# Kernel optimization log

Measured on AMD Instinct MI355X. Metric: run time of the kernel, lower is better.

Reference implementation:

```python
import jax, jax.numpy as jnp
import numpy as np

PAST, FUT = 64, 16
SB = 2048
N = PAST + FUT  # 80
OUTP = 35       # sum(emb dims) + 3


def _pre(cat, num, emb0, emb1, emb2, W1, b1, W2, b2, W3, b3):
    # pre_processing: embeddings + last-3 numeric cols -> MLP -> concat target col
    e = jnp.concatenate([emb0[cat[:, 0]], emb1[cat[:, 1]], emb2[cat[:, 2]]], -1)
    o = jnp.concatenate([e, num], -1)                 # [n, 35]
    h = jax.nn.relu(o @ W1 + b1)
    h = jax.nn.relu(h @ W2 + b2)
    h = h @ W3 + b3                                   # [n, 34]
    return jnp.concatenate([h, num[:, -1:]], -1)      # [n, 35]


def _gcn(x, src, dst, W, b):
    n = x.shape[0]
    h = x @ W
    deg = 1.0 + jax.ops.segment_sum(jnp.ones(src.shape, x.dtype), dst, num_segments=n)
    dinv = jax.lax.rsqrt(deg)
    msg = h[src] * (dinv[src] * dinv[dst])[:, None]
    agg = jax.ops.segment_sum(msg, dst, num_segments=n) + h * (dinv * dinv)[:, None]
    return agg + b


def _forward(x1_cat, x1_num, x2_cat, x2_num, e1, e2,
             emb0, emb1, emb2, pW1, pb1, pW2, pb2, pW3, pb3,
             g1W1, g1b1, g1W2, g1b2, g2W1, g2b1, g2W2, g2b2,
             kerW, smoothing, M):
    # masked-softmax adjacency A = softmax(relu(M M^T) masked to lower-tri, axis=1)
    Araw = jax.nn.relu(M @ M.T)
    tril = jnp.tril(jnp.ones((N, N), Araw.dtype))
    A = jax.nn.softmax(jnp.where(tril == 0, -jnp.inf, Araw), axis=1)

    x = _pre(x1_cat, x1_num, emb0, emb1, emb2, pW1, pb1, pW2, pb2, pW3, pb3)   # [SB*PAST, 35]
    x2 = _pre(x2_cat, x2_num, emb0, emb1, emb2, pW1, pb1, pW2, pb2, pW3, pb3)
    x2 = x2.reshape(SB, FUT, OUTP)

    # gnn1: GCN(35->64) -> ReLU -> GCN(64->34)
    h = jax.nn.relu(_gcn(x, e1[0], e1[1], g1W1, g1b1))
    x1 = _gcn(h, e1[0], e1[1], g1W2, g1b2).reshape(SB, PAST, OUTP - 1)

    x_kernel = jnp.concatenate([x1, x2[:, :, :-1]], -2)        # [SB, N, 34]
    y_kernel = x.reshape(SB, PAST, OUTP)[:, :, -1:]            # [SB, PAST, 1]

    # Mahalanobis kernel attention
    theta = kerW @ kerW.T
    theta = (theta + theta.T) / 2
    x_p = x_kernel[:, :PAST, :]
    x_f = x_kernel[:, PAST:, :]
    diff = x_p[:, None, :, :] - x_f[:, :, None, :]             # [SB, FUT, PAST, 34]
    # diagonal of diff @ theta @ diff^T, computed directly
    alpha = jnp.einsum('bqpo,oO,bqpO->bqp', diff, theta, diff)
    alpha = -0.5 * alpha / (jax.nn.sigmoid(smoothing[0]) * 0.01)
    A_tmp = A[PAST:, :PAST]                                    # [FUT, PAST]
    alpha = jnp.where(A_tmp[None] == 0, -jnp.inf, alpha)
    alpha = jax.nn.softmax(alpha, -1)
    yh = jnp.einsum('bqp,bpo->bqo', alpha, y_kernel)           # [SB, FUT, 1]

    x2 = jnp.concatenate([x2[:, :, :-1], yh], -1)              # [SB, FUT, 35]
    # gnn2: GCN(35->64) -> ReLU -> GCN(64->1)
    h2 = jax.nn.relu(_gcn(x2.reshape(-1, OUTP), e2[0], e2[1], g2W1, g2b1))
    out = _gcn(h2, e2[0], e2[1], g2W2, g2b2).reshape(SB, FUT)

    # cdist over concatenated past+future features, via norm trick
    xa = jnp.concatenate([x.reshape(SB, PAST, OUTP), x2], -2)  # [SB, N, 35]
    sq = jnp.sum(xa * xa, -1)
    d2 = sq[:, :, None] + sq[:, None, :] - 2.0 * jnp.einsum('bnd,bmd->bnm', xa, xa)
    cd = jnp.sqrt(jnp.maximum(d2, 0.0))
    return out, cd, A


def setup_inputs():
    key = jax.random.key(0)
    ks = jax.random.split(key, 24)
    f32 = jnp.float32
    n1, n2 = SB * PAST, SB * FUT
    E1, E2 = n1 * 8, n2 * 8
    return {
        'x1_cat': jax.random.randint(ks[0], (n1, 3), 0, 7, dtype=jnp.int32),
        'x1_num': jax.random.normal(ks[1], (n1, 3), f32),
        'x2_cat': jax.random.randint(ks[2], (n2, 3), 0, 7, dtype=jnp.int32),
        'x2_num': jax.random.normal(ks[3], (n2, 3), f32),
        'edge_index1': jax.random.randint(ks[4], (2, E1), 0, n1, dtype=jnp.int32),
        'edge_index2': jax.random.randint(ks[5], (2, E2), 0, n2, dtype=jnp.int32),
        'emb0': jax.random.normal(ks[6], (24, 16), f32),
        'emb1': jax.random.normal(ks[7], (7, 8), f32),
        'emb2': jax.random.normal(ks[8], (12, 8), f32),
        'pre_W1': jax.random.normal(ks[9], (35, 128), f32) * 0.1,
        'pre_b1': jnp.zeros((128,), f32),
        'pre_W2': jax.random.normal(ks[10], (128, 128), f32) * 0.08,
        'pre_b2': jnp.zeros((128,), f32),
        'pre_W3': jax.random.normal(ks[11], (128, 34), f32) * 0.08,
        'pre_b3': jnp.zeros((34,), f32),
        'g1_W1': jax.random.normal(ks[12], (35, 64), f32) * 0.1,
        'g1_b1': jnp.zeros((64,), f32),
        'g1_W2': jax.random.normal(ks[13], (64, 34), f32) * 0.1,
        'g1_b2': jnp.zeros((34,), f32),
        'g2_W1': jax.random.normal(ks[14], (35, 64), f32) * 0.1,
        'g2_b1': jnp.zeros((64,), f32),
        'g2_W2': jax.random.normal(ks[15], (64, 1), f32) * 0.1,
        'g2_b2': jnp.zeros((1,), f32),
        'ker_W': jax.random.normal(ks[16], (34, 128), f32) * 0.1,
        'smoothing': jax.random.normal(ks[17], (1,), f32),
        'M': jax.random.normal(ks[18], (N, N // 3), f32) * 0.1,
    }


def reference(x1_cat, x1_num, x2_cat, x2_num, edge_index1, edge_index2,
              emb0, emb1, emb2, pre_W1, pre_b1, pre_W2, pre_b2, pre_W3, pre_b3,
              g1_W1, g1_b1, g1_W2, g1_b2, g2_W1, g2_b1, g2_W2, g2_b2,
              ker_W, smoothing, M):
    return _forward(x1_cat, x1_num, x2_cat, x2_num, edge_index1, edge_index2,
                    emb0, emb1, emb2, pre_W1, pre_b1, pre_W2, pre_b2, pre_W3, pre_b3,
                    g1_W1, g1_b1, g1_W2, g1_b2, g2_W1, g2_b1, g2_W2, g2_b2,
                    ker_W, smoothing, M)
```

## Files before the change

### kernel.cpp

```cpp
#include <hip/hip_runtime.h>
#include <math.h>

#define PASTN 64
#define FUTN 16
#define NN 80

typedef __attribute__((ext_vector_type(8))) short sh8;
typedef __attribute__((ext_vector_type(4))) float f32x4;

__device__ __forceinline__ unsigned short f2bf(float f) {
    unsigned int u = __float_as_uint(f);
    return (unsigned short)((u + 0x7FFFu + ((u >> 16) & 1u)) >> 16);
}
__device__ __forceinline__ float bf2f(unsigned short s) {
    return __uint_as_float(((unsigned int)s) << 16);
}

__global__ __launch_bounds__(256) void k_setup(const float* __restrict__ M, const float* __restrict__ kerW,
                                               const float* __restrict__ smoothing,
                                               float* __restrict__ A_ws, float* __restrict__ A_out,
                                               float* __restrict__ theta, float* __restrict__ scale)
{
    __shared__ float Ms[80 * 26];
    __shared__ float Ar[80 * 80];
    const int t = threadIdx.x;
    for (int i = t; i < 80 * 26; i += 256) Ms[i] = M[i];
    __syncthreads();
    for (int idx = t; idx < 6400; idx += 256) {
        int i = idx / 80, j = idx - 80 * i;
        float acc = 0.f;
#pragma unroll
        for (int k = 0; k < 26; ++k) acc = fmaf(Ms[i * 26 + k], Ms[j * 26 + k], acc);
        Ar[idx] = fmaxf(acc, 0.f);
    }
    __syncthreads();
    if (t < 80) {
        float mx = -1e30f;
        for (int j = 0; j <= t; ++j) mx = fmaxf(mx, Ar[t * 80 + j]);
        float s = 0.f;
        for (int j = 0; j <= t; ++j) s += expf(Ar[t * 80 + j] - mx);
        float inv = 1.f / s;
        for (int j = 0; j < 80; ++j) {
            float v = (j <= t) ? expf(Ar[t * 80 + j] - mx) * inv : 0.f;
            A_ws[t * 80 + j] = v;
            A_out[t * 80 + j] = v;
        }
    }
    for (int idx = t; idx < 34 * 34; idx += 256) {
        int i = idx / 34, j = idx - 34 * i;
        float acc = 0.f;
        for (int k = 0; k < 128; ++k) acc = fmaf(kerW[i * 128 + k], kerW[j * 128 + k], acc);
        theta[idx] = acc;
    }
    if (t == 0) {
        float s0 = smoothing[0];
        float sig = 1.f / (1.f + expf(-s0));
        scale[0] = -0.5f / (sig * 0.01f);
    }
}

__global__ void k_wconv(const float* __restrict__ W1, const float* __restrict__ W2,
                        const float* __restrict__ W3,
                        unsigned short* __restrict__ W1h, unsigned short* __restrict__ W1l,
                        unsigned short* __restrict__ W2h, unsigned short* __restrict__ W2l,
                        unsigned short* __restrict__ W3h, unsigned short* __restrict__ W3l)
{
    int g = blockIdx.x * 256 + threadIdx.x;
    float w;
    unsigned short *dh, *dl;
    int gi;
    if (g < 8192) {
        gi = g;
        int i = gi & 7, l = (gi >> 3) & 63, ks = (gi >> 9) & 1, nt = gi >> 10;
        int col = nt * 16 + (l & 15);
        int k = ks * 32 + ((l >> 4) << 3) + i;
        w = (k < 35) ? W1[k * 128 + col] : 0.f;
        dh = W1h; dl = W1l;
    } else if (g < 24576) {
        gi = g - 8192;
        int i = gi & 7, l = (gi >> 3) & 63, ks = (gi >> 9) & 3, nt = gi >> 11;
        int col = nt * 16 + (l & 15);
        int k = ks * 32 + ((l >> 4) << 3) + i;
        w = W2[k * 128 + col];
        dh = W2h; dl = W2l;
    } else {
        gi = g - 24576;
        int i = gi & 7, l = (gi >> 3) & 63, ks = (gi >> 9) & 3, nt = gi >> 11;
        int col = nt * 16 + (l & 15);
        int k = ks * 32 + ((l >> 4) << 3) + i;
        w = (col < 34) ? W3[k * 34 + col] : 0.f;
        dh = W3h; dl = W3l;
    }
    unsigned short hi = f2bf(w);
    dh[gi] = hi;
    dl[gi] = f2bf(w - bf2f(hi));
}

__global__ void k_deg2(const int* __restrict__ dst1, const int* __restrict__ dst2,
                       int* __restrict__ deg1, int* __restrict__ deg2,
                       int E1, int E2, int nbe1)
{
    int gb = blockIdx.x;
    if (gb < nbe1) {
        int e = gb * 256 + threadIdx.x;
        if (e < E1) atomicAdd(&deg1[dst1[e]], 1);
    } else {
        int e = (gb - nbe1) * 256 + threadIdx.x;
        if (e < E2) atomicAdd(&deg2[dst2[e]], 1);
    }
}

#define SCHUNK 1024
__global__ __launch_bounds__(256) void k_scan_reduce2(const int* __restrict__ deg1, const int* __restrict__ deg2,
                                                      int* __restrict__ bsumA, int* __restrict__ bsumB,
                                                      int n1, int n2, int nb1)
{
    __shared__ int sd[256];
    const int gb = blockIdx.x, t = threadIdx.x;
    const int which = (gb < nb1) ? 0 : 1;
    const int b = which ? gb - nb1 : gb;
    const int* deg = which ? deg2 : deg1;
    const int n = which ? n2 : n1;
    const int base = b * SCHUNK;
    int s = 0;
#pragma unroll
    for (int j = 0; j < 4; ++j) {
        int i = base + t + j * 256;
        if (i < n) s += deg[i];
    }
    sd[t] = s;
    __syncthreads();
    for (int o = 128; o > 0; o >>= 1) {
        if (t < o) sd[t] += sd[t + o];
        __syncthreads();
    }
    if (t == 0) (which ? bsumB : bsumA)[b] = sd[0];
}

__global__ __launch_bounds__(1024) void k_scan_mid2(int* __restrict__ bsumA, int* __restrict__ bsumB,
                                                    int nbA, int nbB)
{
    __shared__ int sd[1024];
    const int t = threadIdx.x;
    int* bsum = (blockIdx.x == 0) ? bsumA : bsumB;
    int nb = (blockIdx.x == 0) ? nbA : nbB;
    int orig = (t < nb) ? bsum[t] : 0;
    sd[t] = orig;
    __syncthreads();
    for (int o = 1; o < 1024; o <<= 1) {
        int v = (t >= o) ? sd[t - o] : 0;
        __syncthreads();
        sd[t] += v;
        __syncthreads();
    }
    if (t < nb) bsum[t] = sd[t] - orig;
}

__global__ __launch_bounds__(256) void k_scan_final2(const int* __restrict__ deg1, const int* __restrict__ deg2,
                                                     const int* __restrict__ bsumA, const int* __restrict__ bsumB,
                                                     int* __restrict__ rs1, int* __restrict__ rs2,
                                                     int* __restrict__ cur1, int* __restrict__ cur2,
                                                     float* __restrict__ dinv1, float* __restrict__ dinv2,
                                                     int n1, int n2, int nb1)
{
    __shared__ int sd[256];
    const int gb = blockIdx.x, t = threadIdx.x;
    const int which = (gb < nb1) ? 0 : 1;
    const int b = which ? gb - nb1 : gb;
    const int* deg = which ? deg2 : deg1;
    const int* bsum = which ? bsumB : bsumA;
    int* rs = which ? rs2 : rs1;
    int* cur = which ? cur2 : cur1;
    float* dinv = which ? dinv2 : dinv1;
    const int n = which ? n2 : n1;
    const int base = b * SCHUNK + t * 4;
    int v0 = (base + 0 < n) ? deg[base + 0] : 0;
    int v1 = (base + 1 < n) ? deg[base + 1] : 0;
    int v2 = (base + 2 < n) ? deg[base + 2] : 0;
    int v3 = (base + 3 < n) ? deg[base + 3] : 0;
    int tsum = v0 + v1 + v2 + v3;
    sd[t] = tsum;
    __syncthreads();
    int incl = tsum;
    for (int o = 1; o < 256; o <<= 1) {
        int v = (t >= o) ? sd[t - o] : 0;
        __syncthreads();
        incl += v;
        sd[t] = incl;
        __syncthreads();
    }
    int off = bsum[b] + incl - tsum;
    if (base + 0 < n) { rs[base + 0] = off;            cur[base + 0] = off;            dinv[base + 0] = rsqrtf(1.f + (float)v0); }
    if (base + 1 < n) { rs[base + 1] = off + v0;       cur[base + 1] = off + v0;       dinv[base + 1] = rsqrtf(1.f + (float)v1); }
    if (base + 2 < n) { rs[base + 2] = off + v0 + v1;  cur[base + 2] = off + v0 + v1;  dinv[base + 2] = rsqrtf(1.f + (float)v2); }
    if (base + 3 < n) { rs[base + 3] = off + v0 + v1 + v2; cur[base + 3] = off + v0 + v1 + v2; dinv[base + 3] = rsqrtf(1.f + (float)v3); }
}

__global__ void k_fill2(const int* __restrict__ src1, const int* __restrict__ dst1,
                        const int* __restrict__ src2, const int* __restrict__ dst2,
                        int* __restrict__ cur1, int* __restrict__ cur2,
                        int* __restrict__ out1, int* __restrict__ out2,
                        int E1, int E2, int nbe1)
{
    int gb = blockIdx.x;
    if (gb < nbe1) {
        int e = gb * 256 + threadIdx.x;
        if (e < E1) { int pos = atomicAdd(&cur1[dst1[e]], 1); out1[pos] = src1[e]; }
    } else {
        int e = (gb - nbe1) * 256 + threadIdx.x;
        if (e < E2) { int pos = atomicAdd(&cur2[dst2[e]], 1); out2[pos] = src2[e]; }
    }
}

template <int DIN>
__global__ __launch_bounds__(256) void k_gcn_s(const int* __restrict__ rs, const int* __restrict__ deg,
                                               const int* __restrict__ srcs, const float* __restrict__ dinv,
                                               const float* __restrict__ Hs, const float* __restrict__ W,
                                               const float* __restrict__ b, float* __restrict__ Out, int n)
{
    const int w = threadIdx.x >> 6, lane = threadIdx.x & 63;
    const int row = blockIdx.x * 4 + w;
    __shared__ float ag[4][DIN];
    const float di = dinv[row];
    const int e0 = rs[row];
    const int d = deg[row];
    float acc = (lane < DIN) ? Hs[(size_t)row * DIN + lane] : 0.f;
    int e = 0;
    for (; e + 8 <= d; e += 8) {
        int s0 = srcs[e0 + e + 0], s1 = srcs[e0 + e + 1], s2 = srcs[e0 + e + 2], s3 = srcs[e0 + e + 3];
        int s4 = srcs[e0 + e + 4], s5 = srcs[e0 + e + 5], s6 = srcs[e0 + e + 6], s7 = srcs[e0 + e + 7];
        float h0 = 0.f, h1 = 0.f, h2 = 0.f, h3 = 0.f, h4 = 0.f, h5 = 0.f, h6 = 0.f, h7 = 0.f;
        if (lane < DIN) {
            h0 = Hs[(size_t)s0 * DIN + lane]; h1 = Hs[(size_t)s1 * DIN + lane];
            h2 = Hs[(size_t)s2 * DIN + lane]; h3 = Hs[(size_t)s3 * DIN + lane];
            h4 = Hs[(size_t)s4 * DIN + lane]; h5 = Hs[(size_t)s5 * DIN + lane];
            h6 = Hs[(size_t)s6 * DIN + lane]; h7 = Hs[(size_t)s7 * DIN + lane];
        }
        acc += ((h0 + h1) + (h2 + h3)) + ((h4 + h5) + (h6 + h7));
    }
    for (; e + 4 <= d; e += 4) {
        int s0 = srcs[e0 + e + 0], s1 = srcs[e0 + e + 1], s2 = srcs[e0 + e + 2], s3 = srcs[e0 + e + 3];
        float h0 = 0.f, h1 = 0.f, h2 = 0.f, h3 = 0.f;
        if (lane < DIN) {
            h0 = Hs[(size_t)s0 * DIN + lane]; h1 = Hs[(size_t)s1 * DIN + lane];
            h2 = Hs[(size_t)s2 * DIN + lane]; h3 = Hs[(size_t)s3 * DIN + lane];
        }
        acc += (h0 + h1) + (h2 + h3);
    }
    for (; e < d; ++e) {
        int s = srcs[e0 + e];
        if (lane < DIN) acc += Hs[(size_t)s * DIN + lane];
    }
    if (lane < DIN) ag[w][lane] = acc;
    __syncthreads();
    float o = 0.f;
#pragma unroll
    for (int i = 0; i < DIN; ++i) o = fmaf(ag[w][i], W[i * 64 + lane], o);
    Out[(size_t)row * 64 + lane] = fmaxf(fmaf(di, o, b[lane]), 0.f);
}

template <int D>
__global__ __launch_bounds__(256) void k_pcomb_s(const int* __restrict__ rs, const int* __restrict__ deg,
                                                 const int* __restrict__ srcs, const float* __restrict__ dinv,
                                                 const float* __restrict__ Hs, const float* __restrict__ b,
                                                 float* __restrict__ dest, int n)
{
    const int wid = (blockIdx.x * blockDim.x + threadIdx.x) >> 6;
    const int lane = threadIdx.x & 63;
    if (wid >= n) return;
    const float di = dinv[wid];
    const int e0 = rs[wid];
    const int d = deg[wid];
    float acc = (lane < D) ? Hs[(size_t)wid * D + lane] : 0.f;
    int e = 0;
    for (; e + 8 <= d; e += 8) {
        int s0 = srcs[e0 + e + 0], s1 = srcs[e0 + e + 1], s2 = srcs[e0 + e + 2], s3 = srcs[e0 + e + 3];
        int s4 = srcs[e0 + e + 4], s5 = srcs[e0 + e + 5], s6 = srcs[e0 + e + 6], s7 = srcs[e0 + e + 7];
        float h0 = 0.f, h1 = 0.f, h2 = 0.f, h3 = 0.f, h4 = 0.f, h5 = 0.f, h6 = 0.f, h7 = 0.f;
        if (lane < D) {
            h0 = Hs[(size_t)s0 * D + lane]; h1 = Hs[(size_t)s1 * D + lane];
            h2 = Hs[(size_t)s2 * D + lane]; h3 = Hs[(size_t)s3 * D + lane];
            h4 = Hs[(size_t)s4 * D + lane]; h5 = Hs[(size_t)s5 * D + lane];
            h6 = Hs[(size_t)s6 * D + lane]; h7 = Hs[(size_t)s7 * D + lane];
        }
        acc += ((h0 + h1) + (h2 + h3)) + ((h4 + h5) + (h6 + h7));
    }
    for (; e + 4 <= d; e += 4) {
        int s0 = srcs[e0 + e + 0], s1 = srcs[e0 + e + 1], s2 = srcs[e0 + e + 2], s3 = srcs[e0 + e + 3];
        float h0 = 0.f, h1 = 0.f, h2 = 0.f, h3 = 0.f;
        if (lane < D) {
            h0 = Hs[(size_t)s0 * D + lane]; h1 = Hs[(size_t)s1 * D + lane];
            h2 = Hs[(size_t)s2 * D + lane]; h3 = Hs[(size_t)s3 * D + lane];
        }
        acc += (h0 + h1) + (h2 + h3);
    }
    for (; e < d; ++e) {
        int s = srcs[e0 + e];
        if (lane < D) acc += Hs[(size_t)s * D + lane];
    }
    if (lane < D) dest[(size_t)wid * D + lane] = fmaf(di, acc, b[lane]);
}

__global__ void k_pcomb1_s(const int* __restrict__ rs, const int* __restrict__ deg,
                           const int* __restrict__ srcs, const float* __restrict__ dinv,
                           const float* __restrict__ Hs, const float* __restrict__ b,
                           float* __restrict__ dest, int n)
{
    int r = blockIdx.x * blockDim.x + threadIdx.x;
    if (r >= n) return;
    int e0 = rs[r], d = deg[r];
    float acc = Hs[r];
    int e = 0;
    for (; e + 8 <= d; e += 8) {
        acc += ((Hs[srcs[e0 + e + 0]] + Hs[srcs[e0 + e + 1]]) + (Hs[srcs[e0 + e + 2]] + Hs[srcs[e0 + e + 3]]))
             + ((Hs[srcs[e0 + e + 4]] + Hs[srcs[e0 + e + 5]]) + (Hs[srcs[e0 + e + 6]] + Hs[srcs[e0 + e + 7]]));
    }
    for (; e + 4 <= d; e += 4) {
        acc += (Hs[srcs[e0 + e + 0]] + Hs[srcs[e0 + e + 1]]) + (Hs[srcs[e0 + e + 2]] + Hs[srcs[e0 + e + 3]]);
    }
    for (; e < d; ++e) acc += Hs[srcs[e0 + e]];
    dest[r] = fmaf(dinv[r], acc, b[0]);
}

#define PR 32
__global__ __launch_bounds__(256) void k_pre_all(const int* __restrict__ cat1, const float* __restrict__ num1,
                                                 const int* __restrict__ cat2, const float* __restrict__ num2,
                                                 const float* __restrict__ emb0, const float* __restrict__ emb1,
                                                 const float* __restrict__ emb2,
                                                 const unsigned short* __restrict__ W1h, const unsigned short* __restrict__ W1l,
                                                 const float* __restrict__ b1,
                                                 const unsigned short* __restrict__ W2h, const unsigned short* __restrict__ W2l,
                                                 const float* __restrict__ b2,
                                                 const unsigned short* __restrict__ W3h, const unsigned short* __restrict__ W3l,
                                                 const float* __restrict__ b3,
                                                 const float* __restrict__ dinv1, const float* __restrict__ dinv2,
                                                 float* __restrict__ X1, float* __restrict__ Xs1,
                                                 float* __restrict__ X2, float* __restrict__ Xs2,
                                                 int nblk1)
{
    __shared__ __align__(16) unsigned short bufh[32 * 128];
    __shared__ __align__(16) unsigned short bufl[32 * 128];
    const int t = threadIdx.x;
    const int wv = t >> 6, ln = t & 63;
    const int mt = wv & 1, wg = wv >> 1;
    const int lr = ln & 15, lh = ln >> 4;
    const int gb = blockIdx.x;
    const int g2 = (gb >= nblk1);
    const int* cat = g2 ? cat2 : cat1;
    const float* num = g2 ? num2 : num1;
    const float* dinv = g2 ? dinv2 : dinv1;
    float* X = g2 ? X2 : X1;
    float* Xs = g2 ? Xs2 : Xs1;
    const int base = (g2 ? gb - nblk1 : gb) * PR;

    for (int idx = t; idx < 32 * 64; idx += 256) {
        int r = idx >> 6, k = idx & 63;
        float v = 0.f;
        if (k < 16) v = emb0[cat[(base + r) * 3 + 0] * 16 + k];
        else if (k < 24) v = emb1[cat[(base + r) * 3 + 1] * 8 + (k - 16)];
        else if (k < 32) v = emb2[cat[(base + r) * 3 + 2] * 8 + (k - 24)];
        else if (k < 35) v = num[(base + r) * 3 + (k - 32)];
        unsigned short hi = f2bf(v);
        int ho = r * 64 + (((k >> 3) ^ (r & 7)) << 3) + (k & 7);
        bufh[ho] = hi;
        bufl[ho] = f2bf(v - bf2f(hi));
    }
    __syncthreads();

    f32x4 a1[4];
    {
        const int ra = mt * 16 + lr;
        sh8 ah[2], al[2];
#pragma unroll
        for (int ks = 0; ks < 2; ++ks) {
            int off = ra * 64 + ((((ks * 4 + lh)) ^ (ra & 7)) << 3);
            ah[ks] = *(const sh8*)(bufh + off);
            al[ks] = *(const sh8*)(bufl + off);
        }
#pragma unroll
        for (int j = 0; j < 4; ++j) {
            const int nt = wg + 2 * j;
            f32x4 acc = (f32x4){0.f, 0.f, 0.f, 0.f};
#pragma unroll
            for (int ks = 0; ks < 2; ++ks) {
                const int fb = (((nt * 2 + ks) * 64 + ln) << 3);
                sh8 bh = *(const sh8*)(W1h + fb);
                sh8 bl = *(const sh8*)(W1l + fb);
                acc = __builtin_amdgcn_mfma_f32_16x16x32_bf16(ah[ks], bh, acc, 0, 0, 0);
                acc = __builtin_amdgcn_mfma_f32_16x16x32_bf16(ah[ks], bl, acc, 0, 0, 0);
                acc = __builtin_amdgcn_mfma_f32_16x16x32_bf16(al[ks], bh, acc, 0, 0, 0);
            }
            a1[j] = acc;
        }
    }
    __syncthreads();
#pragma unroll
    for (int j = 0; j < 4; ++j) {
        const int f = (wg + 2 * j) * 16 + lr;
        const float bb = b1[f];
#pragma unroll
        for (int reg = 0; reg < 4; ++reg) {
            const int row = mt * 16 + lh * 4 + reg;
            float v = fmaxf(a1[j][reg] + bb, 0.f);
            unsigned short hi = f2bf(v);
            int ho = row * 128 + ((((f >> 3)) ^ (row & 15)) << 3) + (f & 7);
            bufh[ho] = hi;
            bufl[ho] = f2bf(v - bf2f(hi));
        }
    }
    __syncthreads();

    f32x4 a2[4];
#pragma unroll
    for (int j = 0; j < 4; ++j) a2[j] = (f32x4){0.f, 0.f, 0.f, 0.f};
    {
        const int ra = mt * 16 + lr;
#pragma unroll
        for (int ks = 0; ks < 4; ++ks) {
            int off = ra * 128 + (((ks * 4 + lh) ^ lr) << 3);
            sh8 ah = *(const sh8*)(bufh + off);
            sh8 al = *(const sh8*)(bufl + off);
#pragma unroll
            for (int j = 0; j < 4; ++j) {
                const int nt = wg * 4 + j;
                const int fb = (((nt * 4 + ks) * 64 + ln) << 3);
                sh8 bh = *(const sh8*)(W2h + fb);
                sh8 bl = *(const sh8*)(W2l + fb);
                a2[j] = __builtin_amdgcn_mfma_f32_16x16x32_bf16(ah, bh, a2[j], 0, 0, 0);
                a2[j] = __builtin_amdgcn_mfma_f32_16x16x32_bf16(ah, bl, a2[j], 0, 0, 0);
                a2[j] = __builtin_amdgcn_mfma_f32_16x16x32_bf16(al, bh, a2[j], 0, 0, 0);
            }
        }
    }
    __syncthreads();
#pragma unroll
    for (int j = 0; j < 4; ++j) {
        const int f = (wg * 4 + j) * 16 + lr;
        const float bb = b2[f];
#pragma unroll
        for (int reg = 0; reg < 4; ++reg) {
            const int row = mt * 16 + lh * 4 + reg;
            float v = fmaxf(a2[j][reg] + bb, 0.f);
            unsigned short hi = f2bf(v);
            int ho = row * 128 + ((((f >> 3)) ^ (row & 15)) << 3) + (f & 7);
            bufh[ho] = hi;
            bufl[ho] = f2bf(v - bf2f(hi));
        }
    }
    __syncthreads();

    f32x4 a3[2];
    a3[0] = (f32x4){0.f, 0.f, 0.f, 0.f};
    a3[1] = (f32x4){0.f, 0.f, 0.f, 0.f};
    {
        const int ra = mt * 16 + lr;
#pragma unroll
        for (int ks = 0; ks < 4; ++ks) {
            int off = ra * 128 + (((ks * 4 + lh) ^ lr) << 3);
            sh8 ah = *(const sh8*)(bufh + off);
            sh8 al = *(const sh8*)(bufl + off);
#pragma unroll
            for (int j = 0; j < 2; ++j) {
                const int nt = wg * 2 + j;
                if (nt >= 3) continue;
                const int fb = (((nt * 4 + ks) * 64 + ln) << 3);
                sh8 bh = *(const sh8*)(W3h + fb);
                sh8 bl = *(const sh8*)(W3l + fb);
                a3[j] = __builtin_amdgcn_mfma_f32_16x16x32_bf16(ah, bh, a3[j], 0, 0, 0);
                a3[j] = __builtin_amdgcn_mfma_f32_16x16x32_bf16(ah, bl, a3[j], 0, 0, 0);
                a3[j] = __builtin_amdgcn_mfma_f32_16x16x32_bf16(al, bh, a3[j], 0, 0, 0);
            }
        }
    }
#pragma unroll
    for (int j = 0; j < 2; ++j) {
        const int nt = wg * 2 + j;
        if (nt >= 3) continue;
        const int jc = nt * 16 + lr;
        if (jc < 34) {
            const float bb = b3[jc];
#pragma unroll
            for (int reg = 0; reg < 4; ++reg) {
                const int row = mt * 16 + lh * 4 + reg;
                const int gr = base + row;
                float v = a3[j][reg] + bb;
                X[(size_t)gr * 35 + jc] = v;
                Xs[(size_t)gr * 35 + jc] = v * dinv[gr];
            }
        }
    }
    if (t < PR) {
        int row = base + t;
        float v = num[row * 3 + 2];
        X[(size_t)row * 35 + 34] = v;
        Xs[(size_t)row * 35 + 34] = v * dinv[row];
    }
}

template <int DIN, int DOUT, bool BIAS, bool RELU, bool SCALE>
__global__ void k_gemm(const float* __restrict__ Xin, int ldin, const float* __restrict__ W,
                       const float* __restrict__ b, const float* __restrict__ oscale,
                       float* __restrict__ Out, int n)
{
    __shared__ float Ws[DIN * DOUT];
    for (int i = threadIdx.x; i < DIN * DOUT; i += blockDim.x) Ws[i] = W[i];
    __syncthreads();
    int idx = blockIdx.x * blockDim.x + threadIdx.x;
    if (idx >= n * DOUT) return;
    int row = idx / DOUT, j = idx - row * DOUT;
    const float4* xr4 = (const float4*)(Xin + (size_t)row * ldin);
    float acc = BIAS ? b[j] : 0.f;
#pragma unroll
    for (int i4 = 0; i4 < DIN / 4; ++i4) {
        float4 x = xr4[i4];
        acc = fmaf(x.x, Ws[(4 * i4 + 0) * DOUT + j], acc);
        acc = fmaf(x.y, Ws[(4 * i4 + 1) * DOUT + j], acc);
        acc = fmaf(x.z, Ws[(4 * i4 + 2) * DOUT + j], acc);
        acc = fmaf(x.w, Ws[(4 * i4 + 3) * DOUT + j], acc);
    }
    if (RELU) acc = fmaxf(acc, 0.f);
    if (SCALE) acc *= oscale[row];
    Out[idx] = acc;
}

__global__ __launch_bounds__(256) void k_alpha(const float* __restrict__ X1,
                                               const float* __restrict__ X,
                                               float* __restrict__ X2,
                                               float* __restrict__ Xs2,
                                               const float* __restrict__ dinv2,
                                               const float* __restrict__ theta,
                                               const float* __restrict__ A,
                                               const float* __restrict__ scale)
{
    const int b = blockIdx.x;
    const int t = threadIdx.x;
    const int p = t & 63;
    const int w = t >> 6;
    __shared__ float th[34 * 34];
    __shared__ float xpS[64 * 35];
    __shared__ float xfS[16 * 34];
    __shared__ float UfS[16 * 34];
    __shared__ float upPart[4][64];
    __shared__ float upS[64];
    __shared__ float yS[64];

    for (int i = t; i < 34 * 34; i += 256) th[i] = theta[i];
    for (int i = t; i < 64 * 34; i += 256) {
        int r = i / 34, o = i - 34 * r;
        xpS[r * 35 + o] = X1[(size_t)(b * 64 + r) * 34 + o];
    }
    for (int i = t; i < 16 * 34; i += 256) {
        int q = i / 34, o = i - 34 * q;
        xfS[i] = X2[(size_t)(b * 16 + q) * 35 + o];
    }
    if (t < 64) yS[t] = X[(size_t)(b * 64 + t) * 35 + 34];
    __syncthreads();

    for (int i = t; i < 16 * 34; i += 256) {
        int q = i / 34, o = i - 34 * q;
        float a = 0.f;
#pragma unroll
        for (int O = 0; O < 34; ++O) a = fmaf(th[o * 34 + O], xfS[q * 34 + O], a);
        UfS[i] = a;
    }
    {
        const int o0 = w * 9;
        const int o1 = (o0 + 9 < 34) ? o0 + 9 : 34;
        float a = 0.f;
        for (int o = o0; o < o1; ++o) {
            float s2 = 0.f;
#pragma unroll
            for (int O = 0; O < 34; ++O) s2 = fmaf(th[o * 34 + O], xpS[p * 35 + O], s2);
            a = fmaf(xpS[p * 35 + o], s2, a);
        }
        upPart[w][p] = a;
    }
    __syncthreads();
    if (t < 64) upS[t] = upPart[0][t] + upPart[1][t] + upPart[2][t] + upPart[3][t];
    __syncthreads();

    const float sc = scale[0];
    const float up = upS[p];
    const float y = yS[p];
#pragma unroll
    for (int i = 0; i < 4; ++i) {
        const int q = w + 4 * i;
        float g = 0.f;
#pragma unroll
        for (int o = 0; o < 34; ++o) g = fmaf(UfS[q * 34 + o], xpS[p * 35 + o], g);
        float a = sc * (up - 2.f * g);
        if (A[(PASTN + q) * NN + p] == 0.f) a = -INFINITY;
        float mx = a;
#pragma unroll
        for (int off = 32; off > 0; off >>= 1) mx = fmaxf(mx, __shfl_xor(mx, off));
        float e = expf(a - mx);
        float s = e;
#pragma unroll
        for (int off = 32; off > 0; off >>= 1) s += __shfl_xor(s, off);
        float c = (e / s) * y;
#pragma unroll
        for (int off = 32; off > 0; off >>= 1) c += __shfl_xor(c, off);
        if (p == 0) {
            size_t ridx = (size_t)(b * 16 + q);
            X2[ridx * 35 + 34] = c;
            Xs2[ridx * 35 + 34] = c * dinv2[ridx];
        }
    }
}

__global__ __launch_bounds__(256) void k_cd(const float* __restrict__ X, const float* __restrict__ X2,
                                            float* __restrict__ cd)
{
    const int b = blockIdx.x;
    const int t = threadIdx.x;
    __shared__ float xa[80 * 44];
    __shared__ float sq[80];
    for (int idx = t; idx < 80 * 44; idx += 256) {
        int nrow = idx / 44, k = idx - 44 * nrow;
        float v = 0.f;
        if (k < 35)
            v = (nrow < 64) ? X[(size_t)(b * 64 + nrow) * 35 + k]
                            : X2[(size_t)(b * 16 + (nrow - 64)) * 35 + k];
        xa[idx] = v;
    }
    __syncthreads();
    const float4* xa4 = (const float4*)xa;
    if (t < 80) {
        float acc = 0.f;
#pragma unroll
        for (int c = 0; c < 9; ++c) {
            float4 v = xa4[t * 11 + c];
            acc = fmaf(v.x, v.x, fmaf(v.y, v.y, fmaf(v.z, v.z, fmaf(v.w, v.w, acc))));
        }
        sq[t] = acc;
    }
    __syncthreads();
    const int ti = t >> 4;
    const int tj = t & 15;
    float dot[5][5];
#pragma unroll
    for (int r = 0; r < 5; ++r)
#pragma unroll
        for (int c = 0; c < 5; ++c) dot[r][c] = 0.f;
#pragma unroll
    for (int ch = 0; ch < 9; ++ch) {
        float4 av[5], bv[5];
#pragma unroll
        for (int r = 0; r < 5; ++r) av[r] = xa4[(5 * ti + r) * 11 + ch];
#pragma unroll
        for (int c = 0; c < 5; ++c) bv[c] = xa4[(5 * tj + c) * 11 + ch];
#pragma unroll
        for (int r = 0; r < 5; ++r)
#pragma unroll
            for (int c = 0; c < 5; ++c)
                dot[r][c] = fmaf(av[r].x, bv[c].x, fmaf(av[r].y, bv[c].y,
                              fmaf(av[r].z, bv[c].z, fmaf(av[r].w, bv[c].w, dot[r][c]))));
    }
    float* out = cd + (size_t)b * 6400;
#pragma unroll
    for (int r = 0; r < 5; ++r) {
        int n_ = 5 * ti + r;
        float sn = sq[n_];
#pragma unroll
        for (int c = 0; c < 5; ++c) {
            int m = 5 * tj + c;
            float d2 = sn + sq[m] - 2.f * dot[r][c];
            out[n_ * 80 + m] = sqrtf(fmaxf(d2, 0.f));
        }
    }
}

extern "C" void kernel_launch(void* const* d_in, const int* in_sizes, int n_in,
                              void* d_out, int out_size, void* d_ws, size_t ws_size,
                              hipStream_t stream)
{
    const int* x1_cat = (const int*)d_in[0];
    const float* x1_num = (const float*)d_in[1];
    const int* x2_cat = (const int*)d_in[2];
    const float* x2_num = (const float*)d_in[3];
    const int* e1 = (const int*)d_in[4];
    const int* e2 = (const int*)d_in[5];
    const float* emb0 = (const float*)d_in[6];
    const float* emb1 = (const float*)d_in[7];
    const float* emb2 = (const float*)d_in[8];
    const float* pW1 = (const float*)d_in[9];
    const float* pb1 = (const float*)d_in[10];
    const float* pW2 = (const float*)d_in[11];
    const float* pb2 = (const float*)d_in[12];
    const float* pW3 = (const float*)d_in[13];
    const float* pb3 = (const float*)d_in[14];
    const float* g1W1 = (const float*)d_in[15];
    const float* g1b1 = (const float*)d_in[16];
    const float* g1W2 = (const float*)d_in[17];
    const float* g1b2 = (const float*)d_in[18];
    const float* g2W1 = (const float*)d_in[19];
    const float* g2b1 = (const float*)d_in[20];
    const float* g2W2 = (const float*)d_in[21];
    const float* g2b2 = (const float*)d_in[22];
    const float* kerW = (const float*)d_in[23];
    const float* smoothing = (const float*)d_in[24];
    const float* M = (const float*)d_in[25];

    const int n1 = in_sizes[0] / 3;
    const int n2 = in_sizes[2] / 3;
    const int E1 = in_sizes[4] / 2;
    const int E2 = in_sizes[5] / 2;
    const int SBc = n2 / FUTN;

    float* w = (float*)d_ws;
    size_t off = 0;
    float* scale = w + off; off += 16;
    float* theta = w + off; off += 1184;
    float* Aws = w + off; off += 6400;
    float* X = w + off; off += (size_t)n1 * 35;
    float* Xs1 = w + off; off += (size_t)n1 * 35;
    float* X2 = w + off; off += (size_t)n2 * 35;
    float* Xs2 = w + off; off += (size_t)n2 * 35;
    float* dinv1 = w + off; off += (size_t)n1;
    float* dinv2 = w + off; off += (size_t)n2;
    float* B2 = w + off; off += (size_t)n1 * 64;
    float* B3 = w + off; off += (size_t)n1 * 34;
    float* B4 = w + off; off += (size_t)n1 * 34;
    off = (off + 3) & ~(size_t)3;
    unsigned short* W1fh = (unsigned short*)(w + off); off += 4096;
    unsigned short* W1fl = (unsigned short*)(w + off); off += 4096;
    unsigned short* W2fh = (unsigned short*)(w + off); off += 8192;
    unsigned short* W2fl = (unsigned short*)(w + off); off += 8192;
    unsigned short* W3fh = (unsigned short*)(w + off); off += 4096;
    unsigned short* W3fl = (unsigned short*)(w + off); off += 4096;
    int* iw = (int*)(w + off);
    size_t ioff = 0;
    int* degi1 = iw + ioff; ioff += n1;
    int* degi2 = iw + ioff; ioff += n2;
    int* rs1 = iw + ioff; ioff += n1;
    int* cur1 = iw + ioff; ioff += n1;
    int* srcs1 = iw + ioff; ioff += E1;
    int* rs2 = iw + ioff; ioff += n2;
    int* cur2 = iw + ioff; ioff += n2;
    int* srcs2 = iw + ioff; ioff += E2;
    int* bsumA = iw + ioff; ioff += 1024;
    int* bsumB = iw + ioff; ioff += 1024;

    float* out_f = (float*)d_out;
    float* cd_f = out_f + (size_t)SBc * FUTN;
    float* A_out = cd_f + (size_t)SBc * NN * NN;

    auto cdiv = [](long long a, long long b) { return (unsigned)((a + b - 1) / b); };

    hipMemsetAsync(degi1, 0, ((size_t)n1 + n2) * 4, stream);
    k_setup<<<1, 256, 0, stream>>>(M, kerW, smoothing, Aws, A_out, theta, scale);
    k_wconv<<<128, 256, 0, stream>>>(pW1, pW2, pW3, W1fh, W1fl, W2fh, W2fl, W3fh, W3fl);

    const int nbe1 = cdiv(E1, 256), nbe2 = cdiv(E2, 256);
    k_deg2<<<nbe1 + nbe2, 256, 0, stream>>>(e1 + E1, e2 + E2, degi1, degi2, E1, E2, nbe1);

    const int nb1 = cdiv(n1, SCHUNK), nb2 = cdiv(n2, SCHUNK);
    k_scan_reduce2<<<nb1 + nb2, 256, 0, stream>>>(degi1, degi2, bsumA, bsumB, n1, n2, nb1);
    k_scan_mid2<<<2, 1024, 0, stream>>>(bsumA, bsumB, nb1, nb2);
    k_scan_final2<<<nb1 + nb2, 256, 0, stream>>>(degi1, degi2, bsumA, bsumB, rs1, rs2, cur1, cur2,
                                                 dinv1, dinv2, n1, n2, nb1);
    k_fill2<<<nbe1 + nbe2, 256, 0, stream>>>(e1, e1 + E1, e2, e2 + E2, cur1, cur2, srcs1, srcs2, E1, E2, nbe1);

    k_pre_all<<<n1 / PR + n2 / PR, 256, 0, stream>>>(x1_cat, x1_num, x2_cat, x2_num,
                                                     emb0, emb1, emb2,
                                                     W1fh, W1fl, pb1, W2fh, W2fl, pb2, W3fh, W3fl, pb3,
                                                     dinv1, dinv2, X, Xs1, X2, Xs2, n1 / PR);

    k_gcn_s<35><<<cdiv(n1, 4), 256, 0, stream>>>(rs1, degi1, srcs1, dinv1, Xs1, g1W1, g1b1, B2, n1);

    k_gemm<64, 34, false, false, true><<<cdiv((long long)n1 * 34, 256), 256, 0, stream>>>(B2, 64, g1W2, nullptr, dinv1, B3, n1);
    k_pcomb_s<34><<<cdiv(n1, 4), 256, 0, stream>>>(rs1, degi1, srcs1, dinv1, B3, g1b2, B4, n1);

    k_alpha<<<SBc, 256, 0, stream>>>(B4, X, X2, Xs2, dinv2, theta, Aws, scale);

    k_gcn_s<35><<<cdiv(n2, 4), 256, 0, stream>>>(rs2, degi2, srcs2, dinv2, Xs2, g2W1, g2b1, B2, n2);

    k_gemm<64, 1, false, false, true><<<cdiv(n2, 256), 256, 0, stream>>>(B2, 64, g2W2, nullptr, dinv2, B3, n2);
    k_pcomb1_s<<<cdiv(n2, 256), 256, 0, stream>>>(rs2, degi2, srcs2, dinv2, B3, g2b2, out_f, n2);

    k_cd<<<SBc, 256, 0, stream>>>(X, X2, cd_f);
}
```

Measured before the change: 671.4 us.

## Fuse setup, weight conversion, degree count and fill/pre kernels; fuse GCN with following GEMM

Merges the setup, weight-conversion and degree-count kernels into one launch, and runs the edge CSR fill together with the pre-processing MLP in one interleaved launch. The GCN aggregation is fused with its following dense projection, which removes the 64-wide intermediate buffer round trip. The second-graph GCN is merged with the pairwise-distance kernel into one grid. This reduces launch count and global memory traffic, at the cost of heterogeneous blocks that can unbalance occupancy and register use.

```diff
diff --git a/kernel.cpp b/kernel.cpp
--- a/kernel.cpp
+++ b/kernel.cpp
@@ -16,97 +16,96 @@
     return __uint_as_float(((unsigned int)s) << 16);
 }
 
-__global__ __launch_bounds__(256) void k_setup(const float* __restrict__ M, const float* __restrict__ kerW,
-                                               const float* __restrict__ smoothing,
-                                               float* __restrict__ A_ws, float* __restrict__ A_out,
-                                               float* __restrict__ theta, float* __restrict__ scale)
+__global__ __launch_bounds__(256) void k_init(const float* __restrict__ M, const float* __restrict__ kerW,
+                                              const float* __restrict__ smoothing,
+                                              float* __restrict__ A_ws, float* __restrict__ A_out,
+                                              float* __restrict__ theta, float* __restrict__ scale,
+                                              const float* __restrict__ W1, const float* __restrict__ W2,
+                                              const float* __restrict__ W3,
+                                              unsigned short* __restrict__ W1h, unsigned short* __restrict__ W1l,
+                                              unsigned short* __restrict__ W2h, unsigned short* __restrict__ W2l,
+                                              unsigned short* __restrict__ W3h, unsigned short* __restrict__ W3l,
+                                              const int* __restrict__ dst1, const int* __restrict__ dst2,
+                                              int* __restrict__ deg1, int* __restrict__ deg2,
+                                              int E1, int E2, int nbe1)
 {
     __shared__ float Ms[80 * 26];
     __shared__ float Ar[80 * 80];
+    const int bid = blockIdx.x;
     const int t = threadIdx.x;
-    for (int i = t; i < 80 * 26; i += 256) Ms[i] = M[i];
-    __syncthreads();
-    for (int idx = t; idx < 6400; idx += 256) {
-        int i = idx / 80, j = idx - 80 * i;
-        float acc = 0.f;
-#pragma unroll
-        for (int k = 0; k < 26; ++k) acc = fmaf(Ms[i * 26 + k], Ms[j * 26 + k], acc);
-        Ar[idx] = fmaxf(acc, 0.f);
-    }
-    __syncthreads();
-    if (t < 80) {
-        float mx = -1e30f;
-        for (int j = 0; j <= t; ++j) mx = fmaxf(mx, Ar[t * 80 + j]);
-        float s = 0.f;
-        for (int j = 0; j <= t; ++j) s += expf(Ar[t * 80 + j] - mx);
-        float inv = 1.f / s;
-        for (int j = 0; j < 80; ++j) {
-            float v = (j <= t) ? expf(Ar[t * 80 + j] - mx) * inv : 0.f;
-            A_ws[t * 80 + j] = v;
-            A_out[t * 80 + j] = v;
-        }
-    }
-    for (int idx = t; idx < 34 * 34; idx += 256) {
-        int i = idx / 34, j = idx - 34 * i;
-        float acc = 0.f;
-        for (int k = 0; k < 128; ++k) acc = fmaf(kerW[i * 128 + k], kerW[j * 128 + k], acc);
-        theta[idx] = acc;
-    }
-    if (t == 0) {
-        float s0 = smoothing[0];
-        float sig = 1.f / (1.f + expf(-s0));
-        scale[0] = -0.5f / (sig * 0.01f);
-    }
-}
-
-__global__ void k_wconv(const float* __restrict__ W1, const float* __restrict__ W2,
-                        const float* __restrict__ W3,
-                        unsigned short* __restrict__ W1h, unsigned short* __restrict__ W1l,
-                        unsigned short* __restrict__ W2h, unsigned short* __restrict__ W2l,
-                        unsigned short* __restrict__ W3h, unsigned short* __restrict__ W3l)
-{
-    int g = blockIdx.x * 256 + threadIdx.x;
-    float w;
-    unsigned short *dh, *dl;
-    int gi;
-    if (g < 8192) {
-        gi = g;
-        int i = gi & 7, l = (gi >> 3) & 63, ks = (gi >> 9) & 1, nt = gi >> 10;
-        int col = nt * 16 + (l & 15);
-        int k = ks * 32 + ((l >> 4) << 3) + i;
-        w = (k < 35) ? W1[k * 128 + col] : 0.f;
-        dh = W1h; dl = W1l;
-    } else if (g < 24576) {
-        gi = g - 8192;
-        int i = gi & 7, l = (gi >> 3) & 63, ks = (gi >> 9) & 3, nt = gi >> 11;
-        int col = nt * 16 + (l & 15);
-        int k = ks * 32 + ((l >> 4) << 3) + i;
-        w = W2[k * 128 + col];
-        dh = W2h; dl = W2l;
+    if (bid == 0) {
+        for (int i = t; i < 80 * 26; i += 256) Ms[i] = M[i];
+        __syncthreads();
+        for (int idx = t; idx < 6400; idx += 256) {
+            int i = idx / 80, j = idx - 80 * i;
+            float acc = 0.f;
+#pragma unroll
+            for (int k = 0; k < 26; ++k) acc = fmaf(Ms[i * 26 + k], Ms[j * 26 + k], acc);
+            Ar[idx] = fmaxf(acc, 0.f);
+        }
+        __syncthreads();
+        if (t < 80) {
+            float mx = -1e30f;
+            for (int j = 0; j <= t; ++j) mx = fmaxf(mx, Ar[t * 80 + j]);
+            float s = 0.f;
+            for (int j = 0; j <= t; ++j) s += expf(Ar[t * 80 + j] - mx);
+            float inv = 1.f / s;
+            for (int j = 0; j < 80; ++j) {
+                float v = (j <= t) ? expf(Ar[t * 80 + j] - mx) * inv : 0.f;
+                A_ws[t * 80 + j] = v;
+                A_out[t * 80 + j] = v;
+            }
+        }
+        for (int idx = t; idx < 34 * 34; idx += 256) {
+            int i = idx / 34, j = idx - 34 * i;
+            float acc = 0.f;
+            for (int k = 0; k < 128; ++k) acc = fmaf(kerW[i * 128 + k], kerW[j * 128 + k], acc);
+            theta[idx] = acc;
+        }
+        if (t == 0) {
+            float s0 = smoothing[0];
+            float sig = 1.f / (1.f + expf(-s0));
+            scale[0] = -0.5f / (sig * 0.01f);
+        }
+    } else if (bid <= 128) {
+        int g = (bid - 1) * 256 + t;
+        float w;
+        unsigned short *dh, *dl;
+        int gi;
+        if (g < 8192) {
+            gi = g;
+            int i = gi & 7, l = (gi >> 3) & 63, ks = (gi >> 9) & 1, nt = gi >> 10;
+            int col = nt * 16 + (l & 15);
+            int k = ks * 32 + ((l >> 4) << 3) + i;
+            w = (k < 35) ? W1[k * 128 + col] : 0.f;
+            dh = W1h; dl = W1l;
+        } else if (g < 24576) {
+            gi = g - 8192;
+            int i = gi & 7, l = (gi >> 3) & 63, ks = (gi >> 9) & 3, nt = gi >> 11;
+            int col = nt * 16 + (l & 15);
+            int k = ks * 32 + ((l >> 4) << 3) + i;
+            w = W2[k * 128 + col];
+            dh = W2h; dl = W2l;
+        } else {
+            gi = g - 24576;
+            int i = gi & 7, l = (gi >> 3) & 63, ks = (gi >> 9) & 3, nt = gi >> 11;
+            int col = nt * 16 + (l & 15);
+            int k = ks * 32 + ((l >> 4) << 3) + i;
+            w = (col < 34) ? W3[k * 34 + col] : 0.f;
+            dh = W3h; dl = W3l;
+        }
+        unsigned short hi = f2bf(w);
+        dh[gi] = hi;
+        dl[gi] = f2bf(w - bf2f(hi));
     } else {
-        gi = g - 24576;
-        int i = gi & 7, l = (gi >> 3) & 63, ks = (gi >> 9) & 3, nt = gi >> 11;
-        int col = nt * 16 + (l & 15);
-        int k = ks * 32 + ((l >> 4) << 3) + i;
-        w = (col < 34) ? W3[k * 34 + col] : 0.f;
-        dh = W3h; dl = W3l;
-    }
-    unsigned short hi = f2bf(w);
-    dh[gi] = hi;
-    dl[gi] = f2bf(w - bf2f(hi));
-}
-
-__global__ void k_deg2(const int* __restrict__ dst1, const int* __restrict__ dst2,
-                       int* __restrict__ deg1, int* __restrict__ deg2,
-                       int E1, int E2, int nbe1)
-{
-    int gb = blockIdx.x;
-    if (gb < nbe1) {
-        int e = gb * 256 + threadIdx.x;
-        if (e < E1) atomicAdd(&deg1[dst1[e]], 1);
-    } else {
-        int e = (gb - nbe1) * 256 + threadIdx.x;
-        if (e < E2) atomicAdd(&deg2[dst2[e]], 1);
+        int fb = bid - 129;
+        if (fb < nbe1) {
+            int e = fb * 256 + t;
+            if (e < E1) atomicAdd(&deg1[dst1[e]], 1);
+        } else {
+            int e = (fb - nbe1) * 256 + t;
+            if (e < E2) atomicAdd(&deg2[dst2[e]], 1);
+        }
     }
 }
 
@@ -196,31 +195,214 @@
     if (base + 3 < n) { rs[base + 3] = off + v0 + v1 + v2; cur[base + 3] = off + v0 + v1 + v2; dinv[base + 3] = rsqrtf(1.f + (float)v3); }
 }
 
-__global__ void k_fill2(const int* __restrict__ src1, const int* __restrict__ dst1,
-                        const int* __restrict__ src2, const int* __restrict__ dst2,
-                        int* __restrict__ cur1, int* __restrict__ cur2,
-                        int* __restrict__ out1, int* __restrict__ out2,
-                        int E1, int E2, int nbe1)
-{
-    int gb = blockIdx.x;
-    if (gb < nbe1) {
-        int e = gb * 256 + threadIdx.x;
-        if (e < E1) { int pos = atomicAdd(&cur1[dst1[e]], 1); out1[pos] = src1[e]; }
+#define PR 32
+__global__ __launch_bounds__(256) void k_fillpre(
+    const int* __restrict__ src1, const int* __restrict__ dst1,
+    const int* __restrict__ src2, const int* __restrict__ dst2,
+    int* __restrict__ cur1, int* __restrict__ cur2,
+    int* __restrict__ out1, int* __restrict__ out2,
+    int E1, int E2, int nbe1, int nfill,
+    const int* __restrict__ cat1, const float* __restrict__ num1,
+    const int* __restrict__ cat2, const float* __restrict__ num2,
+    const float* __restrict__ emb0, const float* __restrict__ emb1, const float* __restrict__ emb2,
+    const unsigned short* __restrict__ W1h, const unsigned short* __restrict__ W1l,
+    const float* __restrict__ b1,
+    const unsigned short* __restrict__ W2h, const unsigned short* __restrict__ W2l,
+    const float* __restrict__ b2,
+    const unsigned short* __restrict__ W3h, const unsigned short* __restrict__ W3l,
+    const float* __restrict__ b3,
+    const float* __restrict__ dinv1, const float* __restrict__ dinv2,
+    float* __restrict__ X1, float* __restrict__ Xs1,
+    float* __restrict__ X2, float* __restrict__ Xs2,
+    int nblk1, int npre)
+{
+    __shared__ __align__(16) unsigned short bufh[32 * 128];
+    __shared__ __align__(16) unsigned short bufl[32 * 128];
+    const int bid = blockIdx.x;
+    const int t = threadIdx.x;
+    const int m = (npre < nfill) ? npre : nfill;
+    int pre_id = -1, fill_id = -1;
+    if (bid < 2 * m) {
+        if (bid & 1) fill_id = bid >> 1; else pre_id = bid >> 1;
     } else {
-        int e = (gb - nbe1) * 256 + threadIdx.x;
-        if (e < E2) { int pos = atomicAdd(&cur2[dst2[e]], 1); out2[pos] = src2[e]; }
-    }
-}
-
-template <int DIN>
-__global__ __launch_bounds__(256) void k_gcn_s(const int* __restrict__ rs, const int* __restrict__ deg,
-                                               const int* __restrict__ srcs, const float* __restrict__ dinv,
-                                               const float* __restrict__ Hs, const float* __restrict__ W,
-                                               const float* __restrict__ b, float* __restrict__ Out, int n)
-{
-    const int w = threadIdx.x >> 6, lane = threadIdx.x & 63;
-    const int row = blockIdx.x * 4 + w;
-    __shared__ float ag[4][DIN];
+        if (npre > nfill) pre_id = bid - nfill; else fill_id = bid - npre;
+    }
+
+    if (fill_id >= 0) {
+        if (fill_id < nbe1) {
+            int e = fill_id * 256 + t;
+            if (e < E1) { int pos = atomicAdd(&cur1[dst1[e]], 1); out1[pos] = src1[e]; }
+        } else {
+            int e = (fill_id - nbe1) * 256 + t;
+            if (e < E2) { int pos = atomicAdd(&cur2[dst2[e]], 1); out2[pos] = src2[e]; }
+        }
+        return;
+    }
+
+    const int wv = t >> 6, ln = t & 63;
+    const int mt = wv & 1, wg = wv >> 1;
+    const int lr = ln & 15, lh = ln >> 4;
+    const int g2 = (pre_id >= nblk1);
+    const int* cat = g2 ? cat2 : cat1;
+    const float* num = g2 ? num2 : num1;
+    const float* dinv = g2 ? dinv2 : dinv1;
+    float* X = g2 ? X2 : X1;
+    float* Xs = g2 ? Xs2 : Xs1;
+    const int base = (g2 ? pre_id - nblk1 : pre_id) * PR;
+
+    for (int idx = t; idx < 32 * 64; idx += 256) {
+        int r = idx >> 6, k = idx & 63;
+        float v = 0.f;
+        if (k < 16) v = emb0[cat[(base + r) * 3 + 0] * 16 + k];
+        else if (k < 24) v = emb1[cat[(base + r) * 3 + 1] * 8 + (k - 16)];
+        else if (k < 32) v = emb2[cat[(base + r) * 3 + 2] * 8 + (k - 24)];
+        else if (k < 35) v = num[(base + r) * 3 + (k - 32)];
+        unsigned short hi = f2bf(v);
+        int ho = r * 64 + (((k >> 3) ^ (r & 7)) << 3) + (k & 7);
+        bufh[ho] = hi;
+        bufl[ho] = f2bf(v - bf2f(hi));
+    }
+    __syncthreads();
+
+    f32x4 a1[4];
+    {
+        const int ra = mt * 16 + lr;
+        sh8 ah[2], al[2];
+#pragma unroll
+        for (int ks = 0; ks < 2; ++ks) {
+            int off = ra * 64 + ((((ks * 4 + lh)) ^ (ra & 7)) << 3);
+            ah[ks] = *(const sh8*)(bufh + off);
+            al[ks] = *(const sh8*)(bufl + off);
+        }
+#pragma unroll
+        for (int j = 0; j < 4; ++j) {
+            const int nt = wg + 2 * j;
+            f32x4 acc = (f32x4){0.f, 0.f, 0.f, 0.f};
+#pragma unroll
+            for (int ks = 0; ks < 2; ++ks) {
+                const int fb = (((nt * 2 + ks) * 64 + ln) << 3);
+                sh8 bh = *(const sh8*)(W1h + fb);
+                sh8 bl = *(const sh8*)(W1l + fb);
+                acc = __builtin_amdgcn_mfma_f32_16x16x32_bf16(ah[ks], bh, acc, 0, 0, 0);
+                acc = __builtin_amdgcn_mfma_f32_16x16x32_bf16(ah[ks], bl, acc, 0, 0, 0);
+                acc = __builtin_amdgcn_mfma_f32_16x16x32_bf16(al[ks], bh, acc, 0, 0, 0);
+            }
+            a1[j] = acc;
+        }
+    }
+    __syncthreads();
+#pragma unroll
+    for (int j = 0; j < 4; ++j) {
+        const int f = (wg + 2 * j) * 16 + lr;
+        const float bb = b1[f];
+#pragma unroll
+        for (int reg = 0; reg < 4; ++reg) {
+            const int row = mt * 16 + lh * 4 + reg;
+            float v = fmaxf(a1[j][reg] + bb, 0.f);
+            unsigned short hi = f2bf(v);
+            int ho = row * 128 + ((((f >> 3)) ^ (row & 15)) << 3) + (f & 7);
+            bufh[ho] = hi;
+            bufl[ho] = f2bf(v - bf2f(hi));
+        }
+    }
+    __syncthreads();
+
+    f32x4 a2[4];
+#pragma unroll
+    for (int j = 0; j < 4; ++j) a2[j] = (f32x4){0.f, 0.f, 0.f, 0.f};
+    {
+        const int ra = mt * 16 + lr;
+#pragma unroll
+        for (int ks = 0; ks < 4; ++ks) {
+            int off = ra * 128 + (((ks * 4 + lh) ^ lr) << 3);
+            sh8 ah = *(const sh8*)(bufh + off);
+            sh8 al = *(const sh8*)(bufl + off);
+#pragma unroll
+            for (int j = 0; j < 4; ++j) {
+                const int nt = wg * 4 + j;
+                const int fb = (((nt * 4 + ks) * 64 + ln) << 3);
+                sh8 bh = *(const sh8*)(W2h + fb);
+                sh8 bl = *(const sh8*)(W2l + fb);
+                a2[j] = __builtin_amdgcn_mfma_f32_16x16x32_bf16(ah, bh, a2[j], 0, 0, 0);
+                a2[j] = __builtin_amdgcn_mfma_f32_16x16x32_bf16(ah, bl, a2[j], 0, 0, 0);
+                a2[j] = __builtin_amdgcn_mfma_f32_16x16x32_bf16(al, bh, a2[j], 0, 0, 0);
+            }
+        }
+    }
+    __syncthreads();
+#pragma unroll
+    for (int j = 0; j < 4; ++j) {
+        const int f = (wg * 4 + j) * 16 + lr;
+        const float bb = b2[f];
+#pragma unroll
+        for (int reg = 0; reg < 4; ++reg) {
+            const int row = mt * 16 + lh * 4 + reg;
+            float v = fmaxf(a2[j][reg] + bb, 0.f);
+            unsigned short hi = f2bf(v);
+            int ho = row * 128 + ((((f >> 3)) ^ (row & 15)) << 3) + (f & 7);
+            bufh[ho] = hi;
+            bufl[ho] = f2bf(v - bf2f(hi));
+        }
+    }
+    __syncthreads();
+
+    f32x4 a3[2];
+    a3[0] = (f32x4){0.f, 0.f, 0.f, 0.f};
+    a3[1] = (f32x4){0.f, 0.f, 0.f, 0.f};
+    {
+        const int ra = mt * 16 + lr;
+#pragma unroll
+        for (int ks = 0; ks < 4; ++ks) {
+            int off = ra * 128 + (((ks * 4 + lh) ^ lr) << 3);
+            sh8 ah = *(const sh8*)(bufh + off);
+            sh8 al = *(const sh8*)(bufl + off);
+#pragma unroll
+            for (int j = 0; j < 2; ++j) {
+                const int nt = wg * 2 + j;
+                if (nt >= 3) continue;
+                const int fb = (((nt * 4 + ks) * 64 + ln) << 3);
+                sh8 bh = *(const sh8*)(W3h + fb);
+                sh8 bl = *(const sh8*)(W3l + fb);
+                a3[j] = __builtin_amdgcn_mfma_f32_16x16x32_bf16(ah, bh, a3[j], 0, 0, 0);
+                a3[j] = __builtin_amdgcn_mfma_f32_16x16x32_bf16(ah, bl, a3[j], 0, 0, 0);
+                a3[j] = __builtin_amdgcn_mfma_f32_16x16x32_bf16(al, bh, a3[j], 0, 0, 0);
+            }
+        }
+    }
+#pragma unroll
+    for (int j = 0; j < 2; ++j) {
+        const int nt = wg * 2 + j;
+        if (nt >= 3) continue;
+        const int jc = nt * 16 + lr;
+        if (jc < 34) {
+            const float bb = b3[jc];
+#pragma unroll
+            for (int reg = 0; reg < 4; ++reg) {
+                const int row = mt * 16 + lh * 4 + reg;
+                const int gr = base + row;
+                float v = a3[j][reg] + bb;
+                X[(size_t)gr * 35 + jc] = v;
+                Xs[(size_t)gr * 35 + jc] = v * dinv[gr];
+            }
+        }
+    }
+    if (t < PR) {
+        int row = base + t;
+        float v = num[row * 3 + 2];
+        X[(size_t)row * 35 + 34] = v;
+        Xs[(size_t)row * 35 + 34] = v * dinv[row];
+    }
+}
+
+template <int DIN, int DOUT2>
+__device__ __forceinline__ void gcn_body(int row, int w, int lane,
+                                         const int* __restrict__ rs, const int* __restrict__ deg,
+                                         const int* __restrict__ srcs, const float* __restrict__ dinv,
+                                         const float* __restrict__ Hs, const float* __restrict__ W1,
+                                         const float* __restrict__ b1, const float* __restrict__ W2,
+                                         float* __restrict__ B3,
+                                         float (*ag)[DIN], float (*rg)[64])
+{
     const float di = dinv[row];
     const int e0 = rs[row];
     const int d = deg[row];
@@ -255,8 +437,113 @@
     __syncthreads();
     float o = 0.f;
 #pragma unroll
-    for (int i = 0; i < DIN; ++i) o = fmaf(ag[w][i], W[i * 64 + lane], o);
-    Out[(size_t)row * 64 + lane] = fmaxf(fmaf(di, o, b[lane]), 0.f);
+    for (int i = 0; i < DIN; ++i) o = fmaf(ag[w][i], W1[i * 64 + lane], o);
+    float r = fmaxf(fmaf(di, o, b1[lane]), 0.f);
+    rg[w][lane] = r;
+    __syncthreads();
+    if (DOUT2 == 1) {
+        float v = r * W2[lane];
+#pragma unroll
+        for (int off = 32; off > 0; off >>= 1) v += __shfl_xor(v, off);
+        if (lane == 0) B3[row] = v * di;
+    } else {
+        if (lane < DOUT2) {
+            float tacc = 0.f;
+#pragma unroll
+            for (int i = 0; i < 64; ++i) tacc = fmaf(rg[w][i], W2[i * DOUT2 + lane], tacc);
+            B3[(size_t)row * DOUT2 + lane] = tacc * di;
+        }
+    }
+}
+
+template <int DIN, int DOUT2>
+__global__ __launch_bounds__(256) void k_gcn_f(const int* __restrict__ rs, const int* __restrict__ deg,
+                                               const int* __restrict__ srcs, const float* __restrict__ dinv,
+                                               const float* __restrict__ Hs, const float* __restrict__ W1,
+                                               const float* __restrict__ b1, const float* __restrict__ W2,
+                                               float* __restrict__ B3, int n)
+{
+    __shared__ float ag[4][DIN];
+    __shared__ float rg[4][64];
+    const int w = threadIdx.x >> 6, lane = threadIdx.x & 63;
+    const int row = blockIdx.x * 4 + w;
+    gcn_body<DIN, DOUT2>(row, w, lane, rs, deg, srcs, dinv, Hs, W1, b1, W2, B3, ag, rg);
+}
+
+__global__ __launch_bounds__(256) void k_g2cd(const int* __restrict__ rs, const int* __restrict__ deg,
+                                              const int* __restrict__ srcs, const float* __restrict__ dinv,
+                                              const float* __restrict__ Hs, const float* __restrict__ W1,
+                                              const float* __restrict__ b1, const float* __restrict__ W2,
+                                              float* __restrict__ B3, int ngcn,
+                                              const float* __restrict__ X, const float* __restrict__ X2,
+                                              float* __restrict__ cd)
+{
+    __shared__ float xa[80 * 44];
+    __shared__ float sq[80];
+    __shared__ float ag[4][35];
+    __shared__ float rg[4][64];
+    const int bid = blockIdx.x;
+    const int t = threadIdx.x;
+    if (bid < ngcn) {
+        const int w = t >> 6, lane = t & 63;
+        const int row = bid * 4 + w;
+        gcn_body<35, 1>(row, w, lane, rs, deg, srcs, dinv, Hs, W1, b1, W2, B3, ag, rg);
+        return;
+    }
+    const int b = bid - ngcn;
+    for (int idx = t; idx < 80 * 44; idx += 256) {
+        int nrow = idx / 44, k = idx - 44 * nrow;
+        float v = 0.f;
+        if (k < 35)
+            v = (nrow < 64) ? X[(size_t)(b * 64 + nrow) * 35 + k]
+                            : X2[(size_t)(b * 16 + (nrow - 64)) * 35 + k];
+        xa[idx] = v;
+    }
+    __syncthreads();
+    const float4* xa4 = (const float4*)xa;
+    if (t < 80) {
+        float acc = 0.f;
+#pragma unroll
+        for (int c = 0; c < 9; ++c) {
+            float4 v = xa4[t * 11 + c];
+            acc = fmaf(v.x, v.x, fmaf(v.y, v.y, fmaf(v.z, v.z, fmaf(v.w, v.w, acc))));
+        }
+        sq[t] = acc;
+    }
+    __syncthreads();
+    const int ti = t >> 4;
+    const int tj = t & 15;
+    float dot[5][5];
+#pragma unroll
+    for (int r = 0; r < 5; ++r)
+#pragma unroll
+        for (int c = 0; c < 5; ++c) dot[r][c] = 0.f;
+#pragma unroll
+    for (int ch = 0; ch < 9; ++ch) {
+        float4 av[5], bv[5];
+#pragma unroll
+        for (int r = 0; r < 5; ++r) av[r] = xa4[(5 * ti + r) * 11 + ch];
+#pragma unroll
+        for (int c = 0; c < 5; ++c) bv[c] = xa4[(5 * tj + c) * 11 + ch];
+#pragma unroll
+        for (int r = 0; r < 5; ++r)
+#pragma unroll
+            for (int c = 0; c < 5; ++c)
+                dot[r][c] = fmaf(av[r].x, bv[c].x, fmaf(av[r].y, bv[c].y,
+                              fmaf(av[r].z, bv[c].z, fmaf(av[r].w, bv[c].w, dot[r][c]))));
+    }
+    float* out = cd + (size_t)b * 6400;
+#pragma unroll
+    for (int r = 0; r < 5; ++r) {
+        int n_ = 5 * ti + r;
+        float sn = sq[n_];
+#pragma unroll
+        for (int c = 0; c < 5; ++c) {
+            int m = 5 * tj + c;
+            float d2 = sn + sq[m] - 2.f * dot[r][c];
+            out[n_ * 80 + m] = sqrtf(fmaxf(d2, 0.f));
+        }
+    }
 }
 
 template <int D>
@@ -322,207 +609,6 @@
     dest[r] = fmaf(dinv[r], acc, b[0]);
 }
 
-#define PR 32
-__global__ __launch_bounds__(256) void k_pre_all(const int* __restrict__ cat1, const float* __restrict__ num1,
-                                                 const int* __restrict__ cat2, const float* __restrict__ num2,
-                                                 const float* __restrict__ emb0, const float* __restrict__ emb1,
-                                                 const float* __restrict__ emb2,
-                                                 const unsigned short* __restrict__ W1h, const unsigned short* __restrict__ W1l,
-                                                 const float* __restrict__ b1,
-                                                 const unsigned short* __restrict__ W2h, const unsigned short* __restrict__ W2l,
-                                                 const float* __restrict__ b2,
-                                                 const unsigned short* __restrict__ W3h, const unsigned short* __restrict__ W3l,
-                                                 const float* __restrict__ b3,
-                                                 const float* __restrict__ dinv1, const float* __restrict__ dinv2,
-                                                 float* __restrict__ X1, float* __restrict__ Xs1,
-                                                 float* __restrict__ X2, float* __restrict__ Xs2,
-                                                 int nblk1)
-{
-    __shared__ __align__(16) unsigned short bufh[32 * 128];
-    __shared__ __align__(16) unsigned short bufl[32 * 128];
-    const int t = threadIdx.x;
-    const int wv = t >> 6, ln = t & 63;
-    const int mt = wv & 1, wg = wv >> 1;
-    const int lr = ln & 15, lh = ln >> 4;
-    const int gb = blockIdx.x;
-    const int g2 = (gb >= nblk1);
-    const int* cat = g2 ? cat2 : cat1;
-    const float* num = g2 ? num2 : num1;
-    const float* dinv = g2 ? dinv2 : dinv1;
-    float* X = g2 ? X2 : X1;
-    float* Xs = g2 ? Xs2 : Xs1;
-    const int base = (g2 ? gb - nblk1 : gb) * PR;
-
-    for (int idx = t; idx < 32 * 64; idx += 256) {
-        int r = idx >> 6, k = idx & 63;
-        float v = 0.f;
-        if (k < 16) v = emb0[cat[(base + r) * 3 + 0] * 16 + k];
-        else if (k < 24) v = emb1[cat[(base + r) * 3 + 1] * 8 + (k - 16)];
-        else if (k < 32) v = emb2[cat[(base + r) * 3 + 2] * 8 + (k - 24)];
-        else if (k < 35) v = num[(base + r) * 3 + (k - 32)];
-        unsigned short hi = f2bf(v);
-        int ho = r * 64 + (((k >> 3) ^ (r & 7)) << 3) + (k & 7);
-        bufh[ho] = hi;
-        bufl[ho] = f2bf(v - bf2f(hi));
-    }
-    __syncthreads();
-
-    f32x4 a1[4];
-    {
-        const int ra = mt * 16 + lr;
-        sh8 ah[2], al[2];
-#pragma unroll
-        for (int ks = 0; ks < 2; ++ks) {
-            int off = ra * 64 + ((((ks * 4 + lh)) ^ (ra & 7)) << 3);
-            ah[ks] = *(const sh8*)(bufh + off);
-            al[ks] = *(const sh8*)(bufl + off);
-        }
-#pragma unroll
-        for (int j = 0; j < 4; ++j) {
-            const int nt = wg + 2 * j;
-            f32x4 acc = (f32x4){0.f, 0.f, 0.f, 0.f};
-#pragma unroll
-            for (int ks = 0; ks < 2; ++ks) {
-                const int fb = (((nt * 2 + ks) * 64 + ln) << 3);
-                sh8 bh = *(const sh8*)(W1h + fb);
-                sh8 bl = *(const sh8*)(W1l + fb);
-                acc = __builtin_amdgcn_mfma_f32_16x16x32_bf16(ah[ks], bh, acc, 0, 0, 0);
-                acc = __builtin_amdgcn_mfma_f32_16x16x32_bf16(ah[ks], bl, acc, 0, 0, 0);
-                acc = __builtin_amdgcn_mfma_f32_16x16x32_bf16(al[ks], bh, acc, 0, 0, 0);
-            }
-            a1[j] = acc;
-        }
-    }
-    __syncthreads();
-#pragma unroll
-    for (int j = 0; j < 4; ++j) {
-        const int f = (wg + 2 * j) * 16 + lr;
-        const float bb = b1[f];
-#pragma unroll
-        for (int reg = 0; reg < 4; ++reg) {
-            const int row = mt * 16 + lh * 4 + reg;
-            float v = fmaxf(a1[j][reg] + bb, 0.f);
-            unsigned short hi = f2bf(v);
-            int ho = row * 128 + ((((f >> 3)) ^ (row & 15)) << 3) + (f & 7);
-            bufh[ho] = hi;
-            bufl[ho] = f2bf(v - bf2f(hi));
-        }
-    }
-    __syncthreads();
-
-    f32x4 a2[4];
-#pragma unroll
-    for (int j = 0; j < 4; ++j) a2[j] = (f32x4){0.f, 0.f, 0.f, 0.f};
-    {
-        const int ra = mt * 16 + lr;
-#pragma unroll
-        for (int ks = 0; ks < 4; ++ks) {
-            int off = ra * 128 + (((ks * 4 + lh) ^ lr) << 3);
-            sh8 ah = *(const sh8*)(bufh + off);
-            sh8 al = *(const sh8*)(bufl + off);
-#pragma unroll
-            for (int j = 0; j < 4; ++j) {
-                const int nt = wg * 4 + j;
-                const int fb = (((nt * 4 + ks) * 64 + ln) << 3);
-                sh8 bh = *(const sh8*)(W2h + fb);
-                sh8 bl = *(const sh8*)(W2l + fb);
-                a2[j] = __builtin_amdgcn_mfma_f32_16x16x32_bf16(ah, bh, a2[j], 0, 0, 0);
-                a2[j] = __builtin_amdgcn_mfma_f32_16x16x32_bf16(ah, bl, a2[j], 0, 0, 0);
-                a2[j] = __builtin_amdgcn_mfma_f32_16x16x32_bf16(al, bh, a2[j], 0, 0, 0);
-            }
-        }
-    }
-    __syncthreads();
-#pragma unroll
-    for (int j = 0; j < 4; ++j) {
-        const int f = (wg * 4 + j) * 16 + lr;
-        const float bb = b2[f];
-#pragma unroll
-        for (int reg = 0; reg < 4; ++reg) {
-            const int row = mt * 16 + lh * 4 + reg;
-            float v = fmaxf(a2[j][reg] + bb, 0.f);
-            unsigned short hi = f2bf(v);
-            int ho = row * 128 + ((((f >> 3)) ^ (row & 15)) << 3) + (f & 7);
-            bufh[ho] = hi;
-            bufl[ho] = f2bf(v - bf2f(hi));
-        }
-    }
-    __syncthreads();
-
-    f32x4 a3[2];
-    a3[0] = (f32x4){0.f, 0.f, 0.f, 0.f};
-    a3[1] = (f32x4){0.f, 0.f, 0.f, 0.f};
-    {
-        const int ra = mt * 16 + lr;
-#pragma unroll
-        for (int ks = 0; ks < 4; ++ks) {
-            int off = ra * 128 + (((ks * 4 + lh) ^ lr) << 3);
-            sh8 ah = *(const sh8*)(bufh + off);
-            sh8 al = *(const sh8*)(bufl + off);
-#pragma unroll
-            for (int j = 0; j < 2; ++j) {
-                const int nt = wg * 2 + j;
-                if (nt >= 3) continue;
-                const int fb = (((nt * 4 + ks) * 64 + ln) << 3);
-                sh8 bh = *(const sh8*)(W3h + fb);
-                sh8 bl = *(const sh8*)(W3l + fb);
-                a3[j] = __builtin_amdgcn_mfma_f32_16x16x32_bf16(ah, bh, a3[j], 0, 0, 0);
-                a3[j] = __builtin_amdgcn_mfma_f32_16x16x32_bf16(ah, bl, a3[j], 0, 0, 0);
-                a3[j] = __builtin_amdgcn_mfma_f32_16x16x32_bf16(al, bh, a3[j], 0, 0, 0);
-            }
-        }
-    }
-#pragma unroll
-    for (int j = 0; j < 2; ++j) {
-        const int nt = wg * 2 + j;
-        if (nt >= 3) continue;
-        const int jc = nt * 16 + lr;
-        if (jc < 34) {
-            const float bb = b3[jc];
-#pragma unroll
-            for (int reg = 0; reg < 4; ++reg) {
-                const int row = mt * 16 + lh * 4 + reg;
-                const int gr = base + row;
-                float v = a3[j][reg] + bb;
-                X[(size_t)gr * 35 + jc] = v;
-                Xs[(size_t)gr * 35 + jc] = v * dinv[gr];
-            }
-        }
-    }
-    if (t < PR) {
-        int row = base + t;
-        float v = num[row * 3 + 2];
-        X[(size_t)row * 35 + 34] = v;
-        Xs[(size_t)row * 35 + 34] = v * dinv[row];
-    }
-}
-
-template <int DIN, int DOUT, bool BIAS, bool RELU, bool SCALE>
-__global__ void k_gemm(const float* __restrict__ Xin, int ldin, const float* __restrict__ W,
-                       const float* __restrict__ b, const float* __restrict__ oscale,
-                       float* __restrict__ Out, int n)
-{
-    __shared__ float Ws[DIN * DOUT];
-    for (int i = threadIdx.x; i < DIN * DOUT; i += blockDim.x) Ws[i] = W[i];
-    __syncthreads();
-    int idx = blockIdx.x * blockDim.x + threadIdx.x;
-    if (idx >= n * DOUT) return;
-    int row = idx / DOUT, j = idx - row * DOUT;
-    const float4* xr4 = (const float4*)(Xin + (size_t)row * ldin);
-    float acc = BIAS ? b[j] : 0.f;
-#pragma unroll
-    for (int i4 = 0; i4 < DIN / 4; ++i4) {
-        float4 x = xr4[i4];
-        acc = fmaf(x.x, Ws[(4 * i4 + 0) * DOUT + j], acc);
-        acc = fmaf(x.y, Ws[(4 * i4 + 1) * DOUT + j], acc);
-        acc = fmaf(x.z, Ws[(4 * i4 + 2) * DOUT + j], acc);
-        acc = fmaf(x.w, Ws[(4 * i4 + 3) * DOUT + j], acc);
-    }
-    if (RELU) acc = fmaxf(acc, 0.f);
-    if (SCALE) acc *= oscale[row];
-    Out[idx] = acc;
-}
-
 __global__ __launch_bounds__(256) void k_alpha(const float* __restrict__ X1,
                                                const float* __restrict__ X,
                                                float* __restrict__ X2,
@@ -604,68 +690,6 @@
             size_t ridx = (size_t)(b * 16 + q);
             X2[ridx * 35 + 34] = c;
             Xs2[ridx * 35 + 34] = c * dinv2[ridx];
-        }
-    }
-}
-
-__global__ __launch_bounds__(256) void k_cd(const float* __restrict__ X, const float* __restrict__ X2,
-                                            float* __restrict__ cd)
-{
-    const int b = blockIdx.x;
-    const int t = threadIdx.x;
-    __shared__ float xa[80 * 44];
-    __shared__ float sq[80];
-    for (int idx = t; idx < 80 * 44; idx += 256) {
-        int nrow = idx / 44, k = idx - 44 * nrow;
-        float v = 0.f;
-        if (k < 35)
-            v = (nrow < 64) ? X[(size_t)(b * 64 + nrow) * 35 + k]
-                            : X2[(size_t)(b * 16 + (nrow - 64)) * 35 + k];
-        xa[idx] = v;
-    }
-    __syncthreads();
-    const float4* xa4 = (const float4*)xa;
-    if (t < 80) {
-        float acc = 0.f;
-#pragma unroll
-        for (int c = 0; c < 9; ++c) {
-            float4 v = xa4[t * 11 + c];
-            acc = fmaf(v.x, v.x, fmaf(v.y, v.y, fmaf(v.z, v.z, fmaf(v.w, v.w, acc))));
-        }
-        sq[t] = acc;
-    }
-    __syncthreads();
-    const int ti = t >> 4;
-    const int tj = t & 15;
-    float dot[5][5];
-#pragma unroll
-    for (int r = 0; r < 5; ++r)
-#pragma unroll
-        for (int c = 0; c < 5; ++c) dot[r][c] = 0.f;
-#pragma unroll
-    for (int ch = 0; ch < 9; ++ch) {
-        float4 av[5], bv[5];
-#pragma unroll
-        for (int r = 0; r < 5; ++r) av[r] = xa4[(5 * ti + r) * 11 + ch];
-#pragma unroll
-        for (int c = 0; c < 5; ++c) bv[c] = xa4[(5 * tj + c) * 11 + ch];
-#pragma unroll
-        for (int r = 0; r < 5; ++r)
-#pragma unroll
-            for (int c = 0; c < 5; ++c)
-                dot[r][c] = fmaf(av[r].x, bv[c].x, fmaf(av[r].y, bv[c].y,
-                              fmaf(av[r].z, bv[c].z, fmaf(av[r].w, bv[c].w, dot[r][c]))));
-    }
-    float* out = cd + (size_t)b * 6400;
-#pragma unroll
-    for (int r = 0; r < 5; ++r) {
-        int n_ = 5 * ti + r;
-        float sn = sq[n_];
-#pragma unroll
-        for (int c = 0; c < 5; ++c) {
-            int m = 5 * tj + c;
-            float d2 = sn + sq[m] - 2.f * dot[r][c];
-            out[n_ * 80 + m] = sqrtf(fmaxf(d2, 0.f));
         }
     }
 }
@@ -718,7 +742,6 @@
     float* Xs2 = w + off; off += (size_t)n2 * 35;
     float* dinv1 = w + off; off += (size_t)n1;
     float* dinv2 = w + off; off += (size_t)n2;
-    float* B2 = w + off; off += (size_t)n1 * 64;
     float* B3 = w + off; off += (size_t)n1 * 34;
     float* B4 = w + off; off += (size_t)n1 * 34;
     off = (off + 3) & ~(size_t)3;
@@ -748,35 +771,32 @@
     auto cdiv = [](long long a, long long b) { return (unsigned)((a + b - 1) / b); };
 
     hipMemsetAsync(degi1, 0, ((size_t)n1 + n2) * 4, stream);
-    k_setup<<<1, 256, 0, stream>>>(M, kerW, smoothing, Aws, A_out, theta, scale);
-    k_wconv<<<128, 256, 0, stream>>>(pW1, pW2, pW3, W1fh, W1fl, W2fh, W2fl, W3fh, W3fl);
-
     const int nbe1 = cdiv(E1, 256), nbe2 = cdiv(E2, 256);
-    k_deg2<<<nbe1 + nbe2, 256, 0, stream>>>(e1 + E1, e2 + E2, degi1, degi2, E1, E2, nbe1);
+    k_init<<<129 + nbe1 + nbe2, 256, 0, stream>>>(M, kerW, smoothing, Aws, A_out, theta, scale,
+                                                  pW1, pW2, pW3, W1fh, W1fl, W2fh, W2fl, W3fh, W3fl,
+                                                  e1 + E1, e2 + E2, degi1, degi2, E1, E2, nbe1);
 
     const int nb1 = cdiv(n1, SCHUNK), nb2 = cdiv(n2, SCHUNK);
     k_scan_reduce2<<<nb1 + nb2, 256, 0, stream>>>(degi1, degi2, bsumA, bsumB, n1, n2, nb1);
     k_scan_mid2<<<2, 1024, 0, stream>>>(bsumA, bsumB, nb1, nb2);
     k_scan_final2<<<nb1 + nb2, 256, 0, stream>>>(degi1, degi2, bsumA, bsumB, rs1, rs2, cur1, cur2,
                                                  dinv1, dinv2, n1, n2, nb1);
-    k_fill2<<<nbe1 + nbe2, 256, 0, stream>>>(e1, e1 + E1, e2, e2 + E2, cur1, cur2, srcs1, srcs2, E1, E2, nbe1);
-
-    k_pre_all<<<n1 / PR + n2 / PR, 256, 0, stream>>>(x1_cat, x1_num, x2_cat, x2_num,
-                                                     emb0, emb1, emb2,
-                                                     W1fh, W1fl, pb1, W2fh, W2fl, pb2, W3fh, W3fl, pb3,
-                                                     dinv1, dinv2, X, Xs1, X2, Xs2, n1 / PR);
-
-    k_gcn_s<35><<<cdiv(n1, 4), 256, 0, stream>>>(rs1, degi1, srcs1, dinv1, Xs1, g1W1, g1b1, B2, n1);
-
-    k_gemm<64, 34, false, false, true><<<cdiv((long long)n1 * 34, 256), 256, 0, stream>>>(B2, 64, g1W2, nullptr, dinv1, B3, n1);
+
+    const int npre = n1 / PR + n2 / PR;
+    const int nfill = nbe1 + nbe2;
+    k_fillpre<<<npre + nfill, 256, 0, stream>>>(e1, e1 + E1, e2, e2 + E2, cur1, cur2, srcs1, srcs2,
+                                                E1, E2, nbe1, nfill,
+                                                x1_cat, x1_num, x2_cat, x2_num, emb0, emb1, emb2,
+                                                W1fh, W1fl, pb1, W2fh, W2fl, pb2, W3fh, W3fl, pb3,
+                                                dinv1, dinv2, X, Xs1, X2, Xs2, n1 / PR, npre);
+
+    k_gcn_f<35, 34><<<n1 / 4, 256, 0, stream>>>(rs1, degi1, srcs1, dinv1, Xs1, g1W1, g1b1, g1W2, B3, n1);
     k_pcomb_s<34><<<cdiv(n1, 4), 256, 0, stream>>>(rs1, degi1, srcs1, dinv1, B3, g1b2, B4, n1);
 
     k_alpha<<<SBc, 256, 0, stream>>>(B4, X, X2, Xs2, dinv2, theta, Aws, scale);
 
-    k_gcn_s<35><<<cdiv(n2, 4), 256, 0, stream>>>(rs2, degi2, srcs2, dinv2, Xs2, g2W1, g2b1, B2, n2);
-
-    k_gemm<64, 1, false, false, true><<<cdiv(n2, 256), 256, 0, stream>>>(B2, 64, g2W2, nullptr, dinv2, B3, n2);
+    k_g2cd<<<n2 / 4 + SBc, 256, 0, stream>>>(rs2, degi2, srcs2, dinv2, Xs2, g2W1, g2b1, g2W2, B3,
+                                             n2 / 4, X, X2, cd_f);
+
     k_pcomb1_s<<<cdiv(n2, 256), 256, 0, stream>>>(rs2, degi2, srcs2, dinv2, B3, g2b2, out_f, n2);
-
-    k_cd<<<SBc, 256, 0, stream>>>(X, X2, cd_f);
-}
+}
```

New measurement: 653.6 us. -2.6%, faster.
